# Performance work log

Measured on AMD Instinct MI355X. Metric: run time of the kernel, lower is better.

The kernel has to match this reference:

```python
import jax, jax.numpy as jnp
import numpy as np
import math

B, F, NB, H1, H2, K = 16384, 64, 64, 128, 128, 3
LN_EPS = 1e-5


def setup_inputs() -> dict:
    key = jax.random.key(0)
    ks = jax.random.split(key, 16)
    x = jax.random.normal(ks[0], (B, F), dtype=jnp.float32)
    # RBF params (per feature): centers init linspace(-3,3), log_widths = log(step)
    centers = jnp.broadcast_to(jnp.linspace(-3.0, 3.0, NB), (F, NB)).astype(jnp.float32)
    step = 6.0 / (NB - 1)
    log_widths = jnp.full((F, NB), math.log(step), dtype=jnp.float32)
    def lin(k, shape, fan_in):
        return jax.random.normal(k, shape, dtype=jnp.float32) / np.sqrt(fan_in)
    W1 = lin(ks[1], (F, NB, H1), NB); b1 = jnp.zeros((F, H1), jnp.float32)
    g1 = jnp.ones((F, H1), jnp.float32); be1 = jnp.zeros((F, H1), jnp.float32)
    W2 = lin(ks[2], (F, H1, H2), H1); b2 = jnp.zeros((F, H2), jnp.float32)
    g2 = jnp.ones((F, H2), jnp.float32); be2 = jnp.zeros((F, H2), jnp.float32)
    Wr = lin(ks[3], (F, NB, H2), NB); br = jnp.zeros((F, H2), jnp.float32)
    att = jnp.zeros((F,), jnp.float32)
    bias = jnp.zeros((H2,), jnp.float32)
    Wpi = lin(ks[4], (H2, K), H2); bpi = jnp.zeros((K,), jnp.float32)
    Wa = lin(ks[5], (H2, K), H2); ba = jnp.zeros((K,), jnp.float32)
    Wb = lin(ks[6], (H2, K), H2); bb = jnp.zeros((K,), jnp.float32)
    return dict(x=x, centers=centers, log_widths=log_widths, W1=W1, b1=b1, g1=g1,
                be1=be1, W2=W2, b2=b2, g2=g2, be2=be2, Wr=Wr, br=br, att=att,
                bias=bias, Wpi=Wpi, bpi=bpi, Wa=Wa, ba=ba, Wb=Wb, bb=bb)


def _layernorm(h, g, b):
    mu = jnp.mean(h, axis=-1, keepdims=True)
    var = jnp.mean((h - mu) ** 2, axis=-1, keepdims=True)
    return (h - mu) * jax.lax.rsqrt(var + LN_EPS) * g + b


def reference(x, centers, log_widths, W1, b1, g1, be1, W2, b2, g2, be2, Wr, br,
              att, bias, Wpi, bpi, Wa, ba, Wb, bb):
    # RBF expansion, feature axis batched: x [B,F] -> [B,F,NB]
    xc = jnp.clip(x, -10.0, 10.0)
    widths = jnp.exp(jnp.clip(log_widths, -5.0, 5.0)) + 0.1  # [F,NB]
    dist = (xc[:, :, None] - centers[None]) / widths[None]
    rbf = jnp.exp(-0.5 * jnp.clip(dist, -10.0, 10.0) ** 2)  # [B,F,NB]
    # per-feature MLP (grouped GEMMs via einsum)
    h = jnp.einsum('bfn,fnh->bfh', rbf, W1) + b1[None]
    h = jax.nn.gelu(_layernorm(h, g1[None], be1[None]), approximate=False)
    h = jnp.einsum('bfh,fhk->bfk', h, W2) + b2[None]
    h = jax.nn.gelu(_layernorm(h, g2[None], be2[None]), approximate=False)
    res = jnp.einsum('bfn,fnh->bfh', rbf, Wr) + br[None]
    stacked = h + 0.1 * res  # [B,F,H2]
    # attention-weighted aggregation over features
    w = jax.nn.softmax(att)
    agg = jnp.einsum('bfh,f->bh', stacked, w) + bias  # [B,H2]
    # mixture-beta head
    pi = jax.nn.softmax(agg @ Wpi + bpi, axis=-1)
    alpha = jnp.clip(jax.nn.softplus(agg @ Wa + ba) + 1.01, 1.01, 100.0)
    beta = jnp.clip(jax.nn.softplus(agg @ Wb + bb) + 1.01, 1.01, 100.0)
    pred = jnp.sum(pi * (alpha / (alpha + beta)), axis=-1)
    return jnp.clip(pred, 0.001, 0.999)
```

## Files before the change

kernel.cpp:

```cpp
#include <hip/hip_runtime.h>
#include <math.h>

#define BQ   16384
#define FQ   64
#define NBQ  64
#define HD   128
#define FG   4
#define FPG  16
#define MT   128
#define NT   512

typedef __attribute__((ext_vector_type(8))) short s16x8;
typedef __attribute__((ext_vector_type(4))) float f32x4;

__device__ __forceinline__ unsigned short f2bf(float x) {
    unsigned int u = __float_as_uint(x);
    return (unsigned short)((u + 0x7FFFu + ((u >> 16) & 1u)) >> 16);
}
__device__ __forceinline__ unsigned short bftr(float x) {
    return (unsigned short)(__float_as_uint(x) >> 16);
}

__device__ __forceinline__ float softplus_stable(float v) {
    return (v > 0.0f) ? (v + log1pf(expf(-v))) : log1pf(expf(v));
}

__device__ __forceinline__ f32x4 gelu4(f32x4 v) {
    const f32x4 v2 = v * v;
    const f32x4 tt = v2 * (-0.07135481f) + (-1.5957691f);
    const f32x4 s  = v * tt;
    f32x4 r;
    r[0] = __fdividef(v[0], 1.0f + __expf(s[0]));
    r[1] = __fdividef(v[1], 1.0f + __expf(s[1]));
    r[2] = __fdividef(v[2], 1.0f + __expf(s[2]));
    r[3] = __fdividef(v[3], 1.0f + __expf(s[3]));
    return r;
}

__device__ __forceinline__ float dppsum16(float x) {
    int t;
    t = __builtin_amdgcn_update_dpp(0, __float_as_int(x), 0xB1,  0xF, 0xF, true);
    x += __int_as_float(t);
    t = __builtin_amdgcn_update_dpp(0, __float_as_int(x), 0x4E,  0xF, 0xF, true);
    x += __int_as_float(t);
    t = __builtin_amdgcn_update_dpp(0, __float_as_int(x), 0x125, 0xF, 0xF, true);
    x += __int_as_float(t);
    t = __builtin_amdgcn_update_dpp(0, __float_as_int(x), 0x129, 0xF, 0xF, true);
    x += __int_as_float(t);
    return x;
}

__device__ __forceinline__ void load16_lds(const unsigned short* g, unsigned short* l) {
    __builtin_amdgcn_global_load_lds(
        (const __attribute__((address_space(1))) unsigned int*)(uintptr_t)g,
        (__attribute__((address_space(3))) unsigned int*)(uintptr_t)l,
        16, 0, 0);
}

__device__ __forceinline__ int hofs(int row, int col) {
    return row * 128 + (col ^ (((row >> 2) & 3) << 4));
}

__global__ void __launch_bounds__(256) prep_misc(
    const float* __restrict__ att, const float* __restrict__ log_widths,
    const float* __restrict__ centers, const float* __restrict__ br,
    const float* __restrict__ bias,
    const float* __restrict__ b1, const float* __restrict__ g1, const float* __restrict__ be1,
    const float* __restrict__ b2, const float* __restrict__ g2, const float* __restrict__ be2,
    float* __restrict__ wsoft, float* __restrict__ crw2, float* __restrict__ rbias,
    float* __restrict__ Pk)
{
    const int t = threadIdx.x;
    if (blockIdx.x == 0) {
        __shared__ float ws[64];
        if (t < 64) {
            float v = att[t];
            float m = v;
#pragma unroll
            for (int s = 32; s >= 1; s >>= 1) m = fmaxf(m, __shfl_xor(m, s, 64));
            float e = expf(v - m);
            float ssum = e;
#pragma unroll
            for (int s = 32; s >= 1; s >>= 1) ssum += __shfl_xor(ssum, s, 64);
            const float w = e / ssum;
            ws[t] = w;
            wsoft[t] = w;
        }
        __syncthreads();
        for (int i = t; i < FQ * NBQ; i += 256) {
            float lw = fminf(fmaxf(log_widths[i], -5.0f), 5.0f);
            const float rw = 1.0f / (expf(lw) + 0.1f);
            ((float2*)crw2)[i] = make_float2(rw, -centers[i] * rw);
        }
        if (t < HD) {
            float s = bias[t];
            for (int f = 0; f < FQ; ++f) s += 0.1f * ws[f] * br[f * HD + t];
            rbias[t] = s;
        }
    } else {
        const int id = (blockIdx.x - 1) * 256 + t;
        if (id < FQ * HD) {
            ((float4*)Pk)[id * 2]     = make_float4(b1[id], g1[id], be1[id], 0.0f);
            ((float4*)Pk)[id * 2 + 1] = make_float4(b2[id], g2[id], be2[id], 0.0f);
        }
    }
}

__global__ void __launch_bounds__(256) prep_swz(
    const float* __restrict__ W1, const float* __restrict__ Wr, const float* __restrict__ W2,
    unsigned short* __restrict__ W1s, unsigned short* __restrict__ Wrs,
    unsigned short* __restrict__ W2s)
{
    const int gid = blockIdx.x * 256 + threadIdx.x;
    const float* W; unsigned short* dst; int K, id;
    if (gid < 65536)       { W = W1; dst = W1s; K = 64;  id = gid; }
    else if (gid < 131072) { W = Wr; dst = Wrs; K = 64;  id = gid - 65536; }
    else                   { W = W2; dst = W2s; K = 128; id = gid - 131072; }
    const int KB = K >> 3;
    const int nn = id & 15;
    const int kb = (id >> 4) % KB;
    const int nt = ((id >> 4) / KB) & 7;
    const int f  = id / (KB * 16 * 8);
    const float* src = W + ((size_t)f * K + kb * 8) * HD + nt * 16 + nn;
    s16x8 o;
#pragma unroll
    for (int j = 0; j < 8; ++j) o[j] = (short)f2bf(src[(size_t)j * HD]);
    *(s16x8*)(dst + (size_t)f * K * HD + ((size_t)(nt * KB + kb) * 16 + nn) * 8) = o;
}

__global__ void __launch_bounds__(256) prep_xtr(const float* __restrict__ x,
                                                float* __restrict__ xT) {
    __shared__ float tile[64][65];
    const int t  = threadIdx.x;
    const int b0 = blockIdx.x * 64;
    {
        const int row = t & 63, cg = (t >> 6) * 16;
        const float4* src = (const float4*)(x + (size_t)(b0 + row) * FQ + cg);
#pragma unroll
        for (int i = 0; i < 4; ++i) {
            const float4 v = src[i];
            tile[row][cg + i * 4 + 0] = v.x;
            tile[row][cg + i * 4 + 1] = v.y;
            tile[row][cg + i * 4 + 2] = v.z;
            tile[row][cg + i * 4 + 3] = v.w;
        }
    }
    __syncthreads();
    {
        const int f = t >> 2, r0 = (t & 3) * 16;
        float* dst = xT + (size_t)f * BQ + b0 + r0;
#pragma unroll
        for (int i = 0; i < 16; ++i) dst[i] = tile[r0 + i][f];
    }
}

__global__ void __launch_bounds__(NT, 4) nam_main(
    const float* __restrict__ crw2,
    const float* __restrict__ xT,
    const unsigned short* __restrict__ W1s,
    const unsigned short* __restrict__ Wrs,
    const unsigned short* __restrict__ W2s,
    const float* __restrict__ Pk,
    const float* __restrict__ wsoft,
    float* __restrict__ agg)
{
    __shared__ __align__(16) unsigned short wbuf[16384];
    __shared__ __align__(16) unsigned short hbuf[16384];

    const int t    = threadIdx.x;
    const int ln   = t & 63;
    const int wv   = t >> 6;
    const int n    = ln & 15;
    const int q    = ln >> 4;
    const int wrow = wv * 16;
    const int fg   = blockIdx.x & 3;
    const int rb   = blockIdx.x >> 2;
    const int b0   = rb * MT;

    f32x4 acc[8];
#pragma unroll
    for (int nt = 0; nt < 8; ++nt) acc[nt] = f32x4{0.f, 0.f, 0.f, 0.f};

    for (int ff = 0; ff < FPG; ++ff) {
        const int f = fg * FPG + ((ff + rb) & (FPG - 1));
        __syncthreads();

        {
            const unsigned short* gw1 = W1s + (size_t)f * 8192;
            const unsigned short* gwr = Wrs + (size_t)f * 8192;
#pragma unroll
            for (int i = 0; i < 4; ++i) {
                const int chunk = i * 8 + wv;
                const unsigned short* src = (chunk < 16) ? (gw1 + chunk * 512)
                                                         : (gwr + (chunk - 16) * 512);
                load16_lds(src + ln * 8, wbuf + chunk * 512);
            }
        }

        s16x8 a0, a1;
        {
            float xv = xT[(size_t)f * BQ + b0 + wrow + n];
            xv = fminf(fmaxf(xv, -10.0f), 10.0f);
            const float4* c4 = ((const float4*)crw2) + f * 32;
            unsigned int p[8];
#pragma unroll
            for (int h = 0; h < 2; ++h) {
#pragma unroll
                for (int i = 0; i < 4; ++i) {
                    const float4 cc = c4[h * 16 + q * 4 + i];
                    const float d0 = fmaf(xv, cc.x, cc.y);
                    const float d1 = fmaf(xv, cc.z, cc.w);
                    const float e0 = __expf(-0.5f * d0 * d0);
                    const float e1 = __expf(-0.5f * d1 * d1);
                    p[h * 4 + i] = __builtin_amdgcn_perm(__float_as_uint(e1),
                                                         __float_as_uint(e0), 0x07060302u);
                }
            }
            int4 pa = make_int4(p[0], p[1], p[2], p[3]);
            int4 pb = make_int4(p[4], p[5], p[6], p[7]);
            a0 = *(s16x8*)&pa;
            a1 = *(s16x8*)&pb;
        }
        const float wf   = wsoft[f];
        const float wf01 = 0.1f * wf;
        __syncthreads();

        f32x4 hc[8];
#pragma unroll
        for (int nt = 0; nt < 8; ++nt) {
            const s16x8 bA = *(const s16x8*)&wbuf[(nt * 8 + 0) * 128 + ln * 8];
            const s16x8 bB = *(const s16x8*)&wbuf[(nt * 8 + 4) * 128 + ln * 8];
            f32x4 z = f32x4{0.f, 0.f, 0.f, 0.f};
            z = __builtin_amdgcn_mfma_f32_16x16x32_bf16(a0, bA, z, 0, 0, 0);
            z = __builtin_amdgcn_mfma_f32_16x16x32_bf16(a1, bB, z, 0, 0, 0);
            hc[nt] = z;
            const s16x8 cA = *(const s16x8*)&wbuf[8192 + (nt * 8 + 0) * 128 + ln * 8];
            const s16x8 cB = *(const s16x8*)&wbuf[8192 + (nt * 8 + 4) * 128 + ln * 8];
            f32x4 y = f32x4{0.f, 0.f, 0.f, 0.f};
            y = __builtin_amdgcn_mfma_f32_16x16x32_bf16(a0, cA, y, 0, 0, 0);
            y = __builtin_amdgcn_mfma_f32_16x16x32_bf16(a1, cB, y, 0, 0, 0);
            acc[nt] = y * wf01 + acc[nt];
        }
        __syncthreads();

        {
            const unsigned short* gw2 = W2s + (size_t)f * 16384;
#pragma unroll
            for (int i = 0; i < 4; ++i) {
                const int chunk = i * 8 + wv;
                load16_lds(gw2 + chunk * 512 + ln * 8, wbuf + chunk * 512);
            }
        }

        const size_t pkb = ((size_t)f * HD + n) * 8;
        f32x4 sm = {0.f, 0.f, 0.f, 0.f}, sq = {0.f, 0.f, 0.f, 0.f};
#pragma unroll
        for (int nt = 0; nt < 8; ++nt) {
            const float4 pA = *(const float4*)(Pk + pkb + nt * 128);
            const f32x4 v = hc[nt] + pA.x;
            hc[nt] = v; sm += v; sq += v * v;
        }
        f32x4 mu4, rs4;
#pragma unroll
        for (int i = 0; i < 4; ++i) {
            const float s  = dppsum16(sm[i]);
            const float qq = dppsum16(sq[i]);
            mu4[i] = s * (1.0f / 128.0f);
            const float var = qq * (1.0f / 128.0f) - mu4[i] * mu4[i];
            rs4[i] = rsqrtf(var + 1e-5f);
        }
#pragma unroll
        for (int nt = 0; nt < 8; ++nt) {
            const float4 pA = *(const float4*)(Pk + pkb + nt * 128);
            const f32x4 sg = rs4 * pA.y;
            const f32x4 y  = (hc[nt] - mu4) * sg + pA.z;
            const f32x4 z  = gelu4(y);
#pragma unroll
            for (int i = 0; i < 4; ++i)
                hbuf[hofs(wrow + q * 4 + i, nt * 16 + n)] = bftr(z[i]);
        }
        __syncthreads();

        s16x8 A2[4];
#pragma unroll
        for (int c = 0; c < 4; ++c)
            A2[c] = *(const s16x8*)&hbuf[hofs(wrow + n, c * 32 + q * 8)];
        f32x4 h2[8];
#pragma unroll
        for (int nt = 0; nt < 8; ++nt) {
            f32x4 z = f32x4{0.f, 0.f, 0.f, 0.f};
#pragma unroll
            for (int c = 0; c < 4; ++c) {
                const s16x8 bF = *(const s16x8*)&wbuf[(nt * 16 + c * 4) * 128 + ln * 8];
                z = __builtin_amdgcn_mfma_f32_16x16x32_bf16(A2[c], bF, z, 0, 0, 0);
            }
            h2[nt] = z;
        }

        sm = f32x4{0.f, 0.f, 0.f, 0.f}; sq = f32x4{0.f, 0.f, 0.f, 0.f};
#pragma unroll
        for (int nt = 0; nt < 8; ++nt) {
            const float4 pB = *(const float4*)(Pk + pkb + nt * 128 + 4);
            const f32x4 v = h2[nt] + pB.x;
            h2[nt] = v; sm += v; sq += v * v;
        }
#pragma unroll
        for (int i = 0; i < 4; ++i) {
            const float s  = dppsum16(sm[i]);
            const float qq = dppsum16(sq[i]);
            mu4[i] = s * (1.0f / 128.0f);
            const float var = qq * (1.0f / 128.0f) - mu4[i] * mu4[i];
            rs4[i] = rsqrtf(var + 1e-5f);
        }
#pragma unroll
        for (int nt = 0; nt < 8; ++nt) {
            const float4 pB = *(const float4*)(Pk + pkb + nt * 128 + 4);
            const f32x4 sg = rs4 * pB.y;
            const f32x4 y  = (h2[nt] - mu4) * sg + pB.z;
            acc[nt] = gelu4(y) * wf + acc[nt];
        }
    }

    float* ap = agg + (size_t)(b0 + wrow + q * 4) * HD + n;
#pragma unroll
    for (int nt = 0; nt < 8; ++nt) {
#pragma unroll
        for (int i = 0; i < 4; ++i) {
            atomicAdd(ap + (size_t)i * HD + nt * 16, acc[nt][i]);
        }
    }
}

__global__ void __launch_bounds__(256) nam_head(
    const float* __restrict__ agg, const float* __restrict__ rbias,
    const float* __restrict__ Wpi, const float* __restrict__ bpi,
    const float* __restrict__ Wa,  const float* __restrict__ ba,
    const float* __restrict__ Wb,  const float* __restrict__ bb,
    float* __restrict__ out)
{
    const int gid  = blockIdx.x * blockDim.x + threadIdx.x;
    const int row  = gid >> 6;
    const int lane = threadIdx.x & 63;
    if (row >= BQ) return;

    const float2 p  = ((const float2*)(agg + (size_t)row * HD))[lane];
    const float2 rb = ((const float2*)rbias)[lane];
    const float ax = p.x + rb.x;
    const float ay = p.y + rb.y;

    const float2* wp = (const float2*)Wpi;
    const float2* wa = (const float2*)Wa;
    const float2* wb = (const float2*)Wb;
    const float2 p01 = wp[lane * 3], p23 = wp[lane * 3 + 1], p45 = wp[lane * 3 + 2];
    const float2 a01 = wa[lane * 3], a23 = wa[lane * 3 + 1], a45 = wa[lane * 3 + 2];
    const float2 b01 = wb[lane * 3], b23 = wb[lane * 3 + 1], b45 = wb[lane * 3 + 2];

    float ppi0 = ax * p01.x + ay * p23.y;
    float ppi1 = ax * p01.y + ay * p45.x;
    float ppi2 = ax * p23.x + ay * p45.y;
    float pa0  = ax * a01.x + ay * a23.y;
    float pa1  = ax * a01.y + ay * a45.x;
    float pa2  = ax * a23.x + ay * a45.y;
    float pb0  = ax * b01.x + ay * b23.y;
    float pb1  = ax * b01.y + ay * b45.x;
    float pb2  = ax * b23.x + ay * b45.y;

#pragma unroll
    for (int s = 32; s >= 1; s >>= 1) {
        ppi0 += __shfl_xor(ppi0, s, 64);
        ppi1 += __shfl_xor(ppi1, s, 64);
        ppi2 += __shfl_xor(ppi2, s, 64);
        pa0  += __shfl_xor(pa0,  s, 64);
        pa1  += __shfl_xor(pa1,  s, 64);
        pa2  += __shfl_xor(pa2,  s, 64);
        pb0  += __shfl_xor(pb0,  s, 64);
        pb1  += __shfl_xor(pb1,  s, 64);
        pb2  += __shfl_xor(pb2,  s, 64);
    }

    if (lane == 0) {
        const float z0 = ppi0 + bpi[0], z1 = ppi1 + bpi[1], z2 = ppi2 + bpi[2];
        const float mz = fmaxf(z0, fmaxf(z1, z2));
        const float e0 = expf(z0 - mz), e1 = expf(z1 - mz), e2 = expf(z2 - mz);
        const float es = e0 + e1 + e2;

        const float al0 = fminf(fmaxf(softplus_stable(pa0 + ba[0]) + 1.01f, 1.01f), 100.0f);
        const float al1 = fminf(fmaxf(softplus_stable(pa1 + ba[1]) + 1.01f, 1.01f), 100.0f);
        const float al2 = fminf(fmaxf(softplus_stable(pa2 + ba[2]) + 1.01f, 1.01f), 100.0f);
        const float bt0 = fminf(fmaxf(softplus_stable(pb0 + bb[0]) + 1.01f, 1.01f), 100.0f);
        const float bt1 = fminf(fmaxf(softplus_stable(pb1 + bb[1]) + 1.01f, 1.01f), 100.0f);
        const float bt2 = fminf(fmaxf(softplus_stable(pb2 + bb[2]) + 1.01f, 1.01f), 100.0f);

        const float pred = (e0 * (al0 / (al0 + bt0))
                          + e1 * (al1 / (al1 + bt1))
                          + e2 * (al2 / (al2 + bt2))) / es;
        out[row] = fminf(fmaxf(pred, 0.001f), 0.999f);
    }
}

extern "C" void kernel_launch(void* const* d_in, const int* in_sizes, int n_in,
                              void* d_out, int out_size, void* d_ws, size_t ws_size,
                              hipStream_t stream) {
    const float* x          = (const float*)d_in[0];
    const float* centers    = (const float*)d_in[1];
    const float* log_widths = (const float*)d_in[2];
    const float* W1   = (const float*)d_in[3];
    const float* b1   = (const float*)d_in[4];
    const float* g1   = (const float*)d_in[5];
    const float* be1  = (const float*)d_in[6];
    const float* W2   = (const float*)d_in[7];
    const float* b2   = (const float*)d_in[8];
    const float* g2   = (const float*)d_in[9];
    const float* be2  = (const float*)d_in[10];
    const float* Wr   = (const float*)d_in[11];
    const float* br   = (const float*)d_in[12];
    const float* att  = (const float*)d_in[13];
    const float* bias = (const float*)d_in[14];
    const float* Wpi  = (const float*)d_in[15];
    const float* bpi  = (const float*)d_in[16];
    const float* Wa   = (const float*)d_in[17];
    const float* ba   = (const float*)d_in[18];
    const float* Wb   = (const float*)d_in[19];
    const float* bb   = (const float*)d_in[20];

    char* ws = (char*)d_ws;
    float*          wsoft = (float*)(ws + 0);
    float*          rbias = (float*)(ws + 1024);
    float*          crw2  = (float*)(ws + 8192);
    float*          Pk    = (float*)(ws + 65536);
    float*          xT    = (float*)(ws + 327680);
    unsigned short* W1s   = (unsigned short*)(ws + 4521984);
    unsigned short* Wrs   = (unsigned short*)(ws + 5570560);
    unsigned short* W2s   = (unsigned short*)(ws + 6619136);
    float*          agg   = (float*)(ws + 8716288);

    prep_misc<<<33, 256, 0, stream>>>(att, log_widths, centers, br, bias,
                                      b1, g1, be1, b2, g2, be2,
                                      wsoft, crw2, rbias, Pk);
    prep_swz<<<1024, 256, 0, stream>>>(W1, Wr, W2, W1s, Wrs, W2s);
    prep_xtr<<<256, 256, 0, stream>>>(x, xT);
    hipMemsetAsync(agg, 0, (size_t)BQ * HD * sizeof(float), stream);

    nam_main<<<(BQ / MT) * FG, NT, 0, stream>>>(crw2, xT, W1s, Wrs, W2s, Pk,
                                                wsoft, agg);

    nam_head<<<BQ / 4, 256, 0, stream>>>(agg, rbias, Wpi, bpi, Wa, ba, Wb, bb,
                                         (float*)d_out);
}
```

Before: 436.8 us.

## Swap MFMA operands to keep hidden activations in registers and double-buffer weights

The MFMA operands are swapped to compute the transpose, so the first layer's output already sits in the register layout the second GEMM needs. This removes the LDS round-trip for the hidden activations, along with one barrier and the cross-lane DPP reductions. Weights are now split into two LDS buffers, so the next feature's W1/Wr and W2 loads are issued while the current feature is still computing. The weight swizzle and the Pk parameter packing are rewritten to match the new layout, which adds indexing complexity and some register pressure.

```diff
diff --git a/kernel.cpp b/kernel.cpp
--- a/kernel.cpp
+++ b/kernel.cpp
@@ -17,8 +17,11 @@
     unsigned int u = __float_as_uint(x);
     return (unsigned short)((u + 0x7FFFu + ((u >> 16) & 1u)) >> 16);
 }
-__device__ __forceinline__ unsigned short bftr(float x) {
-    return (unsigned short)(__float_as_uint(x) >> 16);
+
+__device__ __forceinline__ unsigned cvtpk_bf16(float lo, float hi) {
+    unsigned r;
+    asm("v_cvt_pk_bf16_f32 %0, %1, %2" : "=v"(r) : "v"(lo), "v"(hi));
+    return r;
 }
 
 __device__ __forceinline__ float softplus_stable(float v) {
@@ -37,19 +40,6 @@
     return r;
 }
 
-__device__ __forceinline__ float dppsum16(float x) {
-    int t;
-    t = __builtin_amdgcn_update_dpp(0, __float_as_int(x), 0xB1,  0xF, 0xF, true);
-    x += __int_as_float(t);
-    t = __builtin_amdgcn_update_dpp(0, __float_as_int(x), 0x4E,  0xF, 0xF, true);
-    x += __int_as_float(t);
-    t = __builtin_amdgcn_update_dpp(0, __float_as_int(x), 0x125, 0xF, 0xF, true);
-    x += __int_as_float(t);
-    t = __builtin_amdgcn_update_dpp(0, __float_as_int(x), 0x129, 0xF, 0xF, true);
-    x += __int_as_float(t);
-    return x;
-}
-
 __device__ __forceinline__ void load16_lds(const unsigned short* g, unsigned short* l) {
     __builtin_amdgcn_global_load_lds(
         (const __attribute__((address_space(1))) unsigned int*)(uintptr_t)g,
@@ -57,9 +47,6 @@
         16, 0, 0);
 }
 
-__device__ __forceinline__ int hofs(int row, int col) {
-    return row * 128 + (col ^ (((row >> 2) & 3) << 4));
-}
 
 __global__ void __launch_bounds__(256) prep_misc(
     const float* __restrict__ att, const float* __restrict__ log_widths,
@@ -99,9 +86,14 @@
         }
     } else {
         const int id = (blockIdx.x - 1) * 256 + t;
-        if (id < FQ * HD) {
-            ((float4*)Pk)[id * 2]     = make_float4(b1[id], g1[id], be1[id], 0.0f);
-            ((float4*)Pk)[id * 2 + 1] = make_float4(b2[id], g2[id], be2[id], 0.0f);
+        if (id < FQ * 32) {
+            float4* dst = (float4*)Pk + (size_t)id * 6;
+            dst[0] = ((const float4*)b1)[id];
+            dst[1] = ((const float4*)g1)[id];
+            dst[2] = ((const float4*)be1)[id];
+            dst[3] = ((const float4*)b2)[id];
+            dst[4] = ((const float4*)g2)[id];
+            dst[5] = ((const float4*)be2)[id];
         }
     }
 }
@@ -112,20 +104,34 @@
     unsigned short* __restrict__ W2s)
 {
     const int gid = blockIdx.x * 256 + threadIdx.x;
-    const float* W; unsigned short* dst; int K, id;
-    if (gid < 65536)       { W = W1; dst = W1s; K = 64;  id = gid; }
-    else if (gid < 131072) { W = Wr; dst = Wrs; K = 64;  id = gid - 65536; }
-    else                   { W = W2; dst = W2s; K = 128; id = gid - 131072; }
-    const int KB = K >> 3;
-    const int nn = id & 15;
-    const int kb = (id >> 4) % KB;
-    const int nt = ((id >> 4) / KB) & 7;
-    const int f  = id / (KB * 16 * 8);
-    const float* src = W + ((size_t)f * K + kb * 8) * HD + nt * 16 + nn;
-    s16x8 o;
-#pragma unroll
-    for (int j = 0; j < 8; ++j) o[j] = (short)f2bf(src[(size_t)j * HD]);
-    *(s16x8*)(dst + (size_t)f * K * HD + ((size_t)(nt * KB + kb) * 16 + nn) * 8) = o;
+    const int l = gid & 63;
+    const int r = l & 15;
+    const int sig_base = ((r >> 2) << 3) + (r & 3);
+    if (gid < 131072) {
+        const int id = gid & 65535;
+        const float* W          = (gid < 65536) ? W1 : Wr;
+        unsigned short* dst     = (gid < 65536) ? W1s : Wrs;
+        const int c  = (id >> 6) & 1;
+        const int nt = (id >> 7) & 7;
+        const int f  = id >> 10;
+        const int hrow = ((nt >> 1) << 5) + ((nt & 1) << 2) + sig_base;
+        const float* src = W + ((size_t)(f * 64 + c * 32 + (l >> 4) * 8)) * HD + hrow;
+        s16x8 o;
+#pragma unroll
+        for (int j = 0; j < 8; ++j) o[j] = (short)f2bf(src[(size_t)j * HD]);
+        *(s16x8*)(dst + (size_t)f * 8192 + ((size_t)((nt * 2 + c) * 64 + l)) * 8) = o;
+    } else {
+        const int id = gid - 131072;
+        const int c  = (id >> 6) & 3;
+        const int nt = (id >> 8) & 7;
+        const int f  = id >> 11;
+        const int hrow = ((nt >> 1) << 5) + ((nt & 1) << 2) + sig_base;
+        const float* src = W2 + ((size_t)(f * 128 + c * 32 + (l >> 4) * 8)) * HD + hrow;
+        s16x8 o;
+#pragma unroll
+        for (int j = 0; j < 8; ++j) o[j] = (short)f2bf(src[(size_t)j * HD]);
+        *(s16x8*)(W2s + (size_t)f * 16384 + ((size_t)((nt * 4 + c) * 64 + l)) * 8) = o;
+    }
 }
 
 __global__ void __launch_bounds__(256) prep_xtr(const float* __restrict__ x,
@@ -164,45 +170,54 @@
     const float* __restrict__ wsoft,
     float* __restrict__ agg)
 {
-    __shared__ __align__(16) unsigned short wbuf[16384];
-    __shared__ __align__(16) unsigned short hbuf[16384];
-
-    const int t    = threadIdx.x;
-    const int ln   = t & 63;
-    const int wv   = t >> 6;
-    const int n    = ln & 15;
-    const int q    = ln >> 4;
-    const int wrow = wv * 16;
-    const int fg   = blockIdx.x & 3;
-    const int rb   = blockIdx.x >> 2;
-    const int b0   = rb * MT;
+    __shared__ __align__(16) unsigned short bufA[16384];
+    __shared__ __align__(16) unsigned short bufB[16384];
+
+    const int t  = threadIdx.x;
+    const int ln = t & 63;
+    const int wv = t >> 6;
+    const int n  = ln & 15;
+    const int q  = ln >> 4;
+    const int fb = ln * 8;
+    const int fg = blockIdx.x & 3;
+    const int rb = blockIdx.x >> 2;
+    const int b0 = rb * MT;
 
     f32x4 acc[8];
 #pragma unroll
     for (int nt = 0; nt < 8; ++nt) acc[nt] = f32x4{0.f, 0.f, 0.f, 0.f};
 
+    {
+        const int f0 = fg * FPG + (rb & (FPG - 1));
+        const unsigned short* gw1 = W1s + (size_t)f0 * 8192;
+        const unsigned short* gwr = Wrs + (size_t)f0 * 8192;
+        const unsigned short* gw2 = W2s + (size_t)f0 * 16384;
+#pragma unroll
+        for (int i = 0; i < 4; ++i) {
+            const int chunk = i * 8 + wv;
+            const unsigned short* s1 = (chunk < 16) ? (gw1 + chunk * 512)
+                                                    : (gwr + (chunk - 16) * 512);
+            load16_lds(s1 + fb, bufA + chunk * 512);
+        }
+#pragma unroll
+        for (int i = 0; i < 4; ++i) {
+            const int chunk = i * 8 + wv;
+            load16_lds(gw2 + chunk * 512 + fb, bufB + chunk * 512);
+        }
+    }
+
     for (int ff = 0; ff < FPG; ++ff) {
-        const int f = fg * FPG + ((ff + rb) & (FPG - 1));
-        __syncthreads();
-
-        {
-            const unsigned short* gw1 = W1s + (size_t)f * 8192;
-            const unsigned short* gwr = Wrs + (size_t)f * 8192;
-#pragma unroll
-            for (int i = 0; i < 4; ++i) {
-                const int chunk = i * 8 + wv;
-                const unsigned short* src = (chunk < 16) ? (gw1 + chunk * 512)
-                                                         : (gwr + (chunk - 16) * 512);
-                load16_lds(src + ln * 8, wbuf + chunk * 512);
-            }
-        }
+        const int f  = fg * FPG + ((ff + rb) & (FPG - 1));
+        const int fn = fg * FPG + ((ff + 1 + rb) & (FPG - 1));
+        const float wf   = wsoft[f];
+        const float wf01 = 0.1f * wf;
 
         s16x8 a0, a1;
         {
-            float xv = xT[(size_t)f * BQ + b0 + wrow + n];
+            float xv = xT[(size_t)f * BQ + b0 + wv * 16 + n];
             xv = fminf(fmaxf(xv, -10.0f), 10.0f);
             const float4* c4 = ((const float4*)crw2) + f * 32;
-            unsigned int p[8];
+            unsigned p[8];
 #pragma unroll
             for (int h = 0; h < 2; ++h) {
 #pragma unroll
@@ -221,112 +236,125 @@
             a0 = *(s16x8*)&pa;
             a1 = *(s16x8*)&pb;
         }
-        const float wf   = wsoft[f];
-        const float wf01 = 0.1f * wf;
+
         __syncthreads();
 
         f32x4 hc[8];
 #pragma unroll
         for (int nt = 0; nt < 8; ++nt) {
-            const s16x8 bA = *(const s16x8*)&wbuf[(nt * 8 + 0) * 128 + ln * 8];
-            const s16x8 bB = *(const s16x8*)&wbuf[(nt * 8 + 4) * 128 + ln * 8];
+            const s16x8 w10 = *(const s16x8*)&bufA[(nt * 2 + 0) * 512 + fb];
+            const s16x8 w11 = *(const s16x8*)&bufA[(nt * 2 + 1) * 512 + fb];
             f32x4 z = f32x4{0.f, 0.f, 0.f, 0.f};
-            z = __builtin_amdgcn_mfma_f32_16x16x32_bf16(a0, bA, z, 0, 0, 0);
-            z = __builtin_amdgcn_mfma_f32_16x16x32_bf16(a1, bB, z, 0, 0, 0);
+            z = __builtin_amdgcn_mfma_f32_16x16x32_bf16(w10, a0, z, 0, 0, 0);
+            z = __builtin_amdgcn_mfma_f32_16x16x32_bf16(w11, a1, z, 0, 0, 0);
             hc[nt] = z;
-            const s16x8 cA = *(const s16x8*)&wbuf[8192 + (nt * 8 + 0) * 128 + ln * 8];
-            const s16x8 cB = *(const s16x8*)&wbuf[8192 + (nt * 8 + 4) * 128 + ln * 8];
+            const s16x8 wr0 = *(const s16x8*)&bufA[8192 + (nt * 2 + 0) * 512 + fb];
+            const s16x8 wr1 = *(const s16x8*)&bufA[8192 + (nt * 2 + 1) * 512 + fb];
             f32x4 y = f32x4{0.f, 0.f, 0.f, 0.f};
-            y = __builtin_amdgcn_mfma_f32_16x16x32_bf16(a0, cA, y, 0, 0, 0);
-            y = __builtin_amdgcn_mfma_f32_16x16x32_bf16(a1, cB, y, 0, 0, 0);
+            y = __builtin_amdgcn_mfma_f32_16x16x32_bf16(wr0, a0, y, 0, 0, 0);
+            y = __builtin_amdgcn_mfma_f32_16x16x32_bf16(wr1, a1, y, 0, 0, 0);
             acc[nt] = y * wf01 + acc[nt];
         }
+
+        const float4* pkf = (const float4*)Pk + (size_t)f * 192 + q * 12;
+        f32x4 sm4 = {0.f, 0.f, 0.f, 0.f}, sq4 = {0.f, 0.f, 0.f, 0.f};
+#pragma unroll
+        for (int nt = 0; nt < 8; ++nt) {
+            const f32x4 bg = *(const f32x4*)(pkf + (nt >> 1) * 48 + (nt & 1) * 6);
+            const f32x4 v = hc[nt] + bg;
+            hc[nt] = v; sm4 += v; sq4 += v * v;
+        }
+        float sm = (sm4[0] + sm4[1]) + (sm4[2] + sm4[3]);
+        float sq = (sq4[0] + sq4[1]) + (sq4[2] + sq4[3]);
+        sm += __shfl_xor(sm, 16); sm += __shfl_xor(sm, 32);
+        sq += __shfl_xor(sq, 16); sq += __shfl_xor(sq, 32);
+        const float mu = sm * (1.0f / 128.0f);
+        const float rs = rsqrtf(sq * (1.0f / 128.0f) - mu * mu + 1e-5f);
+
         __syncthreads();
 
-        {
-            const unsigned short* gw2 = W2s + (size_t)f * 16384;
+        if (ff < FPG - 1) {
+            const unsigned short* gw1 = W1s + (size_t)fn * 8192;
+            const unsigned short* gwr = Wrs + (size_t)fn * 8192;
 #pragma unroll
             for (int i = 0; i < 4; ++i) {
                 const int chunk = i * 8 + wv;
-                load16_lds(gw2 + chunk * 512 + ln * 8, wbuf + chunk * 512);
+                const unsigned short* s1 = (chunk < 16) ? (gw1 + chunk * 512)
+                                                        : (gwr + (chunk - 16) * 512);
+                load16_lds(s1 + fb, bufA + chunk * 512);
             }
         }
 
-        const size_t pkb = ((size_t)f * HD + n) * 8;
-        f32x4 sm = {0.f, 0.f, 0.f, 0.f}, sq = {0.f, 0.f, 0.f, 0.f};
-#pragma unroll
-        for (int nt = 0; nt < 8; ++nt) {
-            const float4 pA = *(const float4*)(Pk + pkb + nt * 128);
-            const f32x4 v = hc[nt] + pA.x;
-            hc[nt] = v; sm += v; sq += v * v;
-        }
-        f32x4 mu4, rs4;
-#pragma unroll
-        for (int i = 0; i < 4; ++i) {
-            const float s  = dppsum16(sm[i]);
-            const float qq = dppsum16(sq[i]);
-            mu4[i] = s * (1.0f / 128.0f);
-            const float var = qq * (1.0f / 128.0f) - mu4[i] * mu4[i];
-            rs4[i] = rsqrtf(var + 1e-5f);
-        }
-#pragma unroll
-        for (int nt = 0; nt < 8; ++nt) {
-            const float4 pA = *(const float4*)(Pk + pkb + nt * 128);
-            const f32x4 sg = rs4 * pA.y;
-            const f32x4 y  = (hc[nt] - mu4) * sg + pA.z;
-            const f32x4 z  = gelu4(y);
-#pragma unroll
-            for (int i = 0; i < 4; ++i)
-                hbuf[hofs(wrow + q * 4 + i, nt * 16 + n)] = bftr(z[i]);
-        }
-        __syncthreads();
-
-        s16x8 A2[4];
-#pragma unroll
-        for (int c = 0; c < 4; ++c)
-            A2[c] = *(const s16x8*)&hbuf[hofs(wrow + n, c * 32 + q * 8)];
+        unsigned u[16];
+#pragma unroll
+        for (int nt = 0; nt < 8; ++nt) {
+            const f32x4 gg = *(const f32x4*)(pkf + (nt >> 1) * 48 + (nt & 1) * 6 + 1);
+            const f32x4 bb = *(const f32x4*)(pkf + (nt >> 1) * 48 + (nt & 1) * 6 + 2);
+            const f32x4 y = (hc[nt] - mu) * (gg * rs) + bb;
+            const f32x4 z = gelu4(y);
+            u[nt * 2 + 0] = cvtpk_bf16(z[0], z[1]);
+            u[nt * 2 + 1] = cvtpk_bf16(z[2], z[3]);
+        }
+        s16x8 bfr[4];
+#pragma unroll
+        for (int c = 0; c < 4; ++c) {
+            int4 w = make_int4(u[4 * c], u[4 * c + 1], u[4 * c + 2], u[4 * c + 3]);
+            bfr[c] = *(s16x8*)&w;
+        }
+
         f32x4 h2[8];
 #pragma unroll
         for (int nt = 0; nt < 8; ++nt) {
             f32x4 z = f32x4{0.f, 0.f, 0.f, 0.f};
 #pragma unroll
             for (int c = 0; c < 4; ++c) {
-                const s16x8 bF = *(const s16x8*)&wbuf[(nt * 16 + c * 4) * 128 + ln * 8];
-                z = __builtin_amdgcn_mfma_f32_16x16x32_bf16(A2[c], bF, z, 0, 0, 0);
+                const s16x8 w2f = *(const s16x8*)&bufB[(nt * 4 + c) * 512 + fb];
+                z = __builtin_amdgcn_mfma_f32_16x16x32_bf16(w2f, bfr[c], z, 0, 0, 0);
             }
             h2[nt] = z;
         }
 
-        sm = f32x4{0.f, 0.f, 0.f, 0.f}; sq = f32x4{0.f, 0.f, 0.f, 0.f};
-#pragma unroll
-        for (int nt = 0; nt < 8; ++nt) {
-            const float4 pB = *(const float4*)(Pk + pkb + nt * 128 + 4);
-            const f32x4 v = h2[nt] + pB.x;
-            h2[nt] = v; sm += v; sq += v * v;
-        }
+        __builtin_amdgcn_sched_barrier(0);
+        __builtin_amdgcn_s_barrier();
+        __builtin_amdgcn_sched_barrier(0);
+
+        if (ff < FPG - 1) {
+            const unsigned short* gw2 = W2s + (size_t)fn * 16384;
+#pragma unroll
+            for (int i = 0; i < 4; ++i) {
+                const int chunk = i * 8 + wv;
+                load16_lds(gw2 + chunk * 512 + fb, bufB + chunk * 512);
+            }
+        }
+
+        f32x4 tm4 = {0.f, 0.f, 0.f, 0.f}, tq4 = {0.f, 0.f, 0.f, 0.f};
+#pragma unroll
+        for (int nt = 0; nt < 8; ++nt) {
+            const f32x4 bg = *(const f32x4*)(pkf + (nt >> 1) * 48 + (nt & 1) * 6 + 3);
+            const f32x4 v = h2[nt] + bg;
+            h2[nt] = v; tm4 += v; tq4 += v * v;
+        }
+        float tm = (tm4[0] + tm4[1]) + (tm4[2] + tm4[3]);
+        float tq = (tq4[0] + tq4[1]) + (tq4[2] + tq4[3]);
+        tm += __shfl_xor(tm, 16); tm += __shfl_xor(tm, 32);
+        tq += __shfl_xor(tq, 16); tq += __shfl_xor(tq, 32);
+        const float mu2 = tm * (1.0f / 128.0f);
+        const float rs2 = rsqrtf(tq * (1.0f / 128.0f) - mu2 * mu2 + 1e-5f);
+#pragma unroll
+        for (int nt = 0; nt < 8; ++nt) {
+            const f32x4 gg = *(const f32x4*)(pkf + (nt >> 1) * 48 + (nt & 1) * 6 + 4);
+            const f32x4 bb = *(const f32x4*)(pkf + (nt >> 1) * 48 + (nt & 1) * 6 + 5);
+            const f32x4 y = (h2[nt] - mu2) * (gg * rs2) + bb;
+            acc[nt] = gelu4(y) * wf + acc[nt];
+        }
+    }
+
+    float* ap = agg + (size_t)(b0 + wv * 16 + n) * HD + q * 8;
+#pragma unroll
+    for (int nt = 0; nt < 8; ++nt) {
 #pragma unroll
         for (int i = 0; i < 4; ++i) {
-            const float s  = dppsum16(sm[i]);
-            const float qq = dppsum16(sq[i]);
-            mu4[i] = s * (1.0f / 128.0f);
-            const float var = qq * (1.0f / 128.0f) - mu4[i] * mu4[i];
-            rs4[i] = rsqrtf(var + 1e-5f);
-        }
-#pragma unroll
-        for (int nt = 0; nt < 8; ++nt) {
-            const float4 pB = *(const float4*)(Pk + pkb + nt * 128 + 4);
-            const f32x4 sg = rs4 * pB.y;
-            const f32x4 y  = (h2[nt] - mu4) * sg + pB.z;
-            acc[nt] = gelu4(y) * wf + acc[nt];
-        }
-    }
-
-    float* ap = agg + (size_t)(b0 + wrow + q * 4) * HD + n;
-#pragma unroll
-    for (int nt = 0; nt < 8; ++nt) {
-#pragma unroll
-        for (int i = 0; i < 4; ++i) {
-            atomicAdd(ap + (size_t)i * HD + nt * 16, acc[nt][i]);
+            atomicAdd(ap + ((nt >> 1) << 5) + ((nt & 1) << 2) + i, acc[nt][i]);
         }
     }
 }
@@ -434,9 +462,9 @@
     unsigned short* W2s   = (unsigned short*)(ws + 6619136);
     float*          agg   = (float*)(ws + 8716288);
 
-    prep_misc<<<33, 256, 0, stream>>>(att, log_widths, centers, br, bias,
-                                      b1, g1, be1, b2, g2, be2,
-                                      wsoft, crw2, rbias, Pk);
+    prep_misc<<<9, 256, 0, stream>>>(att, log_widths, centers, br, bias,
+                                     b1, g1, be1, b2, g2, be2,
+                                     wsoft, crw2, rbias, Pk);
     prep_swz<<<1024, 256, 0, stream>>>(W1, Wr, W2, W1s, Wrs, W2s);
     prep_xtr<<<256, 256, 0, stream>>>(x, xT);
     hipMemsetAsync(agg, 0, (size_t)BQ * HD * sizeof(float), stream);
```

After: 668.6 us. 1.53x slower.
